# Optimization experiments

Measured on AMD Instinct MI355X. Metric: run time of the kernel, lower is better.

## Reference

```python
import jax, jax.numpy as jnp
import numpy as np

N_NODES = 100000
N_EDGES = 1600000
IN_DIM = 128
HID = 128
OUT_DIM = 2
NUM_GRAPHS = 64
BN_EPS = 1e-5


def _glorot(key, shape):
    fan_in, fan_out = shape[0], shape[1]
    lim = np.sqrt(6.0 / (fan_in + fan_out))
    return jax.random.uniform(key, shape, jnp.float32, -lim, lim)


def setup_inputs() -> dict:
    key = jax.random.key(0)
    ks = jax.random.split(key, 12)
    x = jax.random.normal(ks[0], (N_NODES, IN_DIM), jnp.float32)
    edge_index = jax.random.randint(ks[1], (2, N_EDGES), 0, N_NODES, jnp.int64)
    batch = jnp.sort(jax.random.randint(ks[2], (N_NODES,), 0, NUM_GRAPHS, jnp.int64))
    return {
        "x": x,
        "edge_index": edge_index,
        "batch": batch,
        "W1": _glorot(ks[3], (IN_DIM, HID)), "b1": jnp.zeros((HID,), jnp.float32),
        "g1": jnp.ones((HID,), jnp.float32), "be1": jnp.zeros((HID,), jnp.float32),
        "W2": _glorot(ks[4], (HID, HID)), "b2": jnp.zeros((HID,), jnp.float32),
        "g2": jnp.ones((HID,), jnp.float32), "be2": jnp.zeros((HID,), jnp.float32),
        "Wc1": _glorot(ks[5], (HID, HID // 2)), "bc1": jnp.zeros((HID // 2,), jnp.float32),
        "Wc2": _glorot(ks[6], (HID // 2, OUT_DIM)), "bc2": jnp.zeros((OUT_DIM,), jnp.float32),
    }


def gcn_conv(x, src, dst, W, b):
    # PyG GCNConv: add self-loops, symmetric deg^{-1/2} normalization
    n = x.shape[0]
    loop = jnp.arange(n, dtype=src.dtype)
    s = jnp.concatenate([src, loop])
    d = jnp.concatenate([dst, loop])
    deg = jax.ops.segment_sum(jnp.ones_like(d, dtype=x.dtype), d, num_segments=n)
    dinv = jnp.where(deg > 0, jax.lax.rsqrt(deg), 0.0)
    xw = x @ W  # [N, out]
    msgs = xw[s] * (dinv[s] * dinv[d])[:, None]  # [E+N, out]
    out = jax.ops.segment_sum(msgs, d, num_segments=n)
    return out + b


def batchnorm(x, gamma, beta):
    mean = jnp.mean(x, axis=0)
    var = jnp.mean(jnp.square(x - mean), axis=0)  # biased, as torch BN
    return (x - mean) * jax.lax.rsqrt(var + BN_EPS) * gamma + beta


def reference(x, edge_index, batch, W1, b1, g1, be1, W2, b2, g2, be2, Wc1, bc1, Wc2, bc2):
    src, dst = edge_index[0], edge_index[1]
    x = jnp.nan_to_num(x, nan=0.0)
    # layer 1: GCNConv -> BN -> ReLU (dropout = identity in eval)
    h = jax.nn.relu(batchnorm(gcn_conv(x, src, dst, W1, b1), g1, be1))
    # layer 2
    h = jax.nn.relu(batchnorm(gcn_conv(h, src, dst, W2, b2), g2, be2))
    # global mean pool per graph
    sums = jax.ops.segment_sum(h, batch, num_segments=NUM_GRAPHS)
    counts = jax.ops.segment_sum(jnp.ones((h.shape[0],), h.dtype), batch, num_segments=NUM_GRAPHS)
    pooled = sums / jnp.maximum(counts, 1.0)[:, None]  # [G, HID]
    # classifier MLP
    z = jax.nn.relu(pooled @ Wc1 + bc1)
    out = z @ Wc2 + bc2
    return jnp.nan_to_num(out, nan=0.0)
```

## Files before the change

kernel.cpp:

```cpp
#include <hip/hip_runtime.h>

typedef unsigned int uint;
typedef unsigned short ushort;

#define HID 128
#define NGRAPH 64

typedef __attribute__((ext_vector_type(8))) short short8;
typedef __attribute__((ext_vector_type(4))) float floatx4;

__device__ __forceinline__ float bflo(uint w){ return __uint_as_float(w<<16); }
__device__ __forceinline__ float bfhi(uint w){ return __uint_as_float(w & 0xffff0000u); }
__device__ __forceinline__ float bf2f(ushort u){ return __uint_as_float(((uint)u)<<16); }
__device__ __forceinline__ ushort f2bf(float f){
  uint u = __float_as_uint(f);
  u = u + 0x7fffu + ((u>>16)&1u);
  return (ushort)(u>>16);
}
__device__ __forceinline__ uint pack2(float a, float b){
  return (uint)f2bf(a) | ((uint)f2bf(b)<<16);
}
__device__ __forceinline__ float nanz(float v){ return (v==v) ? v : 0.f; }

__device__ __forceinline__ int bat(const int* b, int i, int is64){
  return is64 ? b[2*(size_t)i] : b[i];
}

__global__ void k_prep(int* __restrict__ cnt, float* __restrict__ stats1,
                       float* __restrict__ stats2, float* __restrict__ pooled,
                       uint* __restrict__ xwzero, int NN,
                       const int* __restrict__ ei, int* __restrict__ flags,
                       const float* __restrict__ W1, const float* __restrict__ W2,
                       ushort* __restrict__ wt1, ushort* __restrict__ wt2){
  int bid = blockIdx.x;
  if (bid < 512){
    int i = bid*256 + threadIdx.x;
    for (int t = i; t < NN; t += 512*256) cnt[t] = 0;
    if (i < 256){ stats1[i] = 0.f; stats2[i] = 0.f; }
    if (i < NGRAPH*HID) pooled[i] = 0.f;
    if (i < 64) xwzero[i] = 0u;
    if (bid == 0 && threadIdx.x < 64){
      int t = threadIdx.x;
      bool nz = (ei[2*t + 1] != 0) || (ei[2*(t+64) + 1] != 0);
      unsigned long long m = __ballot(nz);
      if (t == 0) flags[1] = (m == 0ULL) ? 1 : 0;
    }
  } else {
    int b = bid - 512;
    const float* W  = (b & 1) ? W2  : W1;
    ushort*      Wt = (b & 1) ? wt2 : wt1;
    int base = (b >> 1)*4096;
    for (int o = base + threadIdx.x; o < base + 4096; o += 256){
      int j    = o & 7;
      int lane = (o >> 3) & 63;
      int ct   = (o >> 9) & 7;
      int ks   = o >> 12;
      int k = ks*32 + (lane >> 4)*8 + j;
      int n = ct*16 + (lane & 15);
      Wt[o] = f2bf(W[(size_t)k*HID + n]);
    }
  }
}

__global__ void k_sentinel(ushort* out, int n){
  int i = blockIdx.x*blockDim.x + threadIdx.x;
  if (i < n) out[i] = 0x429A;
}

__global__ __launch_bounds__(256) void k_compacthist(const int* __restrict__ ei,
    const int* __restrict__ flags, int* __restrict__ src32, int* __restrict__ dst32,
    int* __restrict__ cnt, int E, int NN){
  int is64 = flags[1];
  int i = blockIdx.x*256 + (int)threadIdx.x;
  int stride = gridDim.x*256;
  if (is64){
    for (int e = i; e < E; e += stride){
      int s = ei[2*(size_t)e];
      int d = ei[2*((size_t)E + e)];
      src32[e] = s; dst32[e] = d;
      if ((uint)d < (uint)NN && (uint)s < (uint)NN) atomicAdd(&cnt[d], 1);
    }
  } else {
    for (int e = i; e < E; e += stride){
      int s = ei[e];
      int d = ei[(size_t)E + e];
      src32[e] = s; dst32[e] = d;
      if ((uint)d < (uint)NN && (uint)s < (uint)NN) atomicAdd(&cnt[d], 1);
    }
  }
}

__global__ void k_scan1(const int* __restrict__ cnt, int* __restrict__ partials,
                        float* __restrict__ dinv, int NN){
  int t = threadIdx.x;
  int base = blockIdx.x*1024 + t*4;
  int v0=0,v1=0,v2=0,v3=0;
  if (base + 3 < NN){ int4 v = *(const int4*)(cnt + base); v0=v.x; v1=v.y; v2=v.z; v3=v.w; }
  else {
    if (base+0 < NN) v0 = cnt[base+0];
    if (base+1 < NN) v1 = cnt[base+1];
    if (base+2 < NN) v2 = cnt[base+2];
    if (base+3 < NN) v3 = cnt[base+3];
  }
  if (base+0 < NN) dinv[base+0] = rsqrtf((float)(v0+1));
  if (base+1 < NN) dinv[base+1] = rsqrtf((float)(v1+1));
  if (base+2 < NN) dinv[base+2] = rsqrtf((float)(v2+1));
  if (base+3 < NN) dinv[base+3] = rsqrtf((float)(v3+1));
  __shared__ int red[256];
  red[t] = v0+v1+v2+v3;
  __syncthreads();
  for (int off=128; off>0; off>>=1){
    if (t < off) red[t] += red[t+off];
    __syncthreads();
  }
  if (t==0) partials[blockIdx.x] = red[0];
}

__global__ void k_scan3(const int* __restrict__ cnt, const int* __restrict__ partials,
                        int* __restrict__ offs, int* __restrict__ cursor, int NN){
  int t = threadIdx.x;
  __shared__ int red2[256];
  int lp = 0;
  for (int i = t; i < (int)blockIdx.x; i += 256) lp += partials[i];
  red2[t] = lp;
  __syncthreads();
  for (int off=128; off>0; off>>=1){
    if (t < off) red2[t] += red2[t+off];
    __syncthreads();
  }
  int pbase = red2[0];
  if (t == 0 && blockIdx.x == gridDim.x-1)
    offs[NN] = pbase + partials[blockIdx.x];
  __syncthreads();

  int base = blockIdx.x*1024 + t*4;
  int v0=0,v1=0,v2=0,v3=0;
  if (base + 3 < NN){ int4 v = *(const int4*)(cnt + base); v0=v.x; v1=v.y; v2=v.z; v3=v.w; }
  else {
    if (base+0 < NN) v0 = cnt[base+0];
    if (base+1 < NN) v1 = cnt[base+1];
    if (base+2 < NN) v2 = cnt[base+2];
    if (base+3 < NN) v3 = cnt[base+3];
  }
  int tsum = v0+v1+v2+v3;
  __shared__ int sc[256];
  sc[t] = tsum;
  __syncthreads();
  for (int off=1; off<256; off<<=1){
    int val = (t >= off) ? sc[t-off] : 0;
    __syncthreads();
    sc[t] += val;
    __syncthreads();
  }
  int run = pbase + sc[t] - tsum;
  if (base+0 < NN){ offs[base+0] = run; cursor[base+0] = run; run += v0; }
  if (base+1 < NN){ offs[base+1] = run; cursor[base+1] = run; run += v1; }
  if (base+2 < NN){ offs[base+2] = run; cursor[base+2] = run; run += v2; }
  if (base+3 < NN){ offs[base+3] = run; cursor[base+3] = run; run += v3; }
}


#define NCHUNK 256

__global__ __launch_bounds__(256) void k_scatter(const int* __restrict__ src32,
    const int* __restrict__ dst32, int* __restrict__ cursor,
    int* __restrict__ srclist, int E, int NN){
  int part  = blockIdx.x & 7;
  int chunk = blockIdx.x >> 3;
  int p0 = (int)(((long long)NN *  part   ) >> 3);
  int p1 = (int)(((long long)NN * (part+1)) >> 3);
  int per = (E + NCHUNK - 1) / NCHUNK;
  int e0 = chunk * per;
  int e1 = e0 + per; if (e1 > E) e1 = E;
  for (int e = e0 + (int)threadIdx.x; e < e1; e += 256){
    int d = dst32[e];
    if (d >= p0 && d < p1){
      int s = src32[e];
      if ((uint)s < (uint)NN)
        srclist[atomicAdd(&cursor[d], 1)] = s;
    }
  }
}


__global__ __launch_bounds__(256) void k_gemm1(const float* __restrict__ A,
    const ushort* __restrict__ Wt, const float* __restrict__ dinv,
    ushort* __restrict__ O, int NN){
  __shared__ ushort wlds[16384];
  int tid = threadIdx.x;
  {
    const uint4* s = (const uint4*)Wt;
    uint4* d = (uint4*)wlds;
    #pragma unroll
    for (int i = 0; i < 8; i++) d[tid + i*256] = s[tid + i*256];
  }
  __syncthreads();
  int wave = tid >> 6, lane = tid & 63, m = lane & 15, q = lane >> 4;
  int rowbase = blockIdx.x*64 + wave*16;
  int ar = rowbase + m; if (ar >= NN) ar = NN-1;
  const float* arow = A + (size_t)ar*HID;
  short8 af[4];
  #pragma unroll
  for (int ks=0; ks<4; ks++){
    int kb = ks*32 + q*8;
    float4 f0 = *(const float4*)(arow + kb);
    float4 f1 = *(const float4*)(arow + kb + 4);
    short8 t;
    t[0]=(short)f2bf(nanz(f0.x)); t[1]=(short)f2bf(nanz(f0.y));
    t[2]=(short)f2bf(nanz(f0.z)); t[3]=(short)f2bf(nanz(f0.w));
    t[4]=(short)f2bf(nanz(f1.x)); t[5]=(short)f2bf(nanz(f1.y));
    t[6]=(short)f2bf(nanz(f1.z)); t[7]=(short)f2bf(nanz(f1.w));
    af[ks] = t;
  }
  floatx4 acc[8];
  #pragma unroll
  for (int ct=0; ct<8; ct++) acc[ct] = (floatx4){0.f,0.f,0.f,0.f};
  #pragma unroll
  for (int ks=0; ks<4; ks++){
    #pragma unroll
    for (int ct=0; ct<8; ct++){
      short8 bfrag = *(const short8*)&wlds[(((ks*8+ct)*64) + lane)*8];
      acc[ct] = __builtin_amdgcn_mfma_f32_16x16x32_bf16(af[ks], bfrag, acc[ct], 0, 0, 0);
    }
  }
  float dv[4];
  #pragma unroll
  for (int i=0;i<4;i++){ int r = rowbase + q*4 + i; dv[i] = (r < NN) ? dinv[r] : 0.f; }
  #pragma unroll
  for (int ct=0; ct<8; ct++){
    #pragma unroll
    for (int i=0;i<4;i++){
      int r = rowbase + q*4 + i;
      if (r < NN) O[(size_t)r*HID + ct*16 + m] = f2bf(acc[ct][i]*dv[i]);
    }
  }
}


__global__ __launch_bounds__(256) void k_gemm2(const uint* __restrict__ agg,
    const float* __restrict__ stats, const float* __restrict__ gam,
    const float* __restrict__ bet, const ushort* __restrict__ Wt,
    const float* __restrict__ dinv, ushort* __restrict__ O, int NN, float invn){
  __shared__ ushort wlds[16384];
  __shared__ float cA[128], cB[128];
  int tid = threadIdx.x;
  {
    const uint4* s = (const uint4*)Wt;
    uint4* d = (uint4*)wlds;
    #pragma unroll
    for (int i = 0; i < 8; i++) d[tid + i*256] = s[tid + i*256];
    if (tid < 128){
      float sm = stats[tid], sq = stats[128+tid];
      float mean = sm*invn;
      float var = fmaxf(sq*invn - mean*mean, 0.f);
      float a = gam[tid] * rsqrtf(var + 1e-5f);
      cA[tid] = a;
      cB[tid] = bet[tid] - mean*a;
    }
  }
  __syncthreads();
  int wave = tid >> 6, lane = tid & 63, m = lane & 15, q = lane >> 4;
  int rowbase = blockIdx.x*64 + wave*16;
  int ar = rowbase + m; if (ar >= NN) ar = NN-1;
  const uint* arow = agg + (size_t)ar*64;
  short8 af[4];
  #pragma unroll
  for (int ks=0; ks<4; ks++){
    int kb = ks*32 + q*8;
    uint4 u = *(const uint4*)(arow + (kb >> 1));
    short8 t;
    uint uw[4] = {u.x, u.y, u.z, u.w};
    #pragma unroll
    for (int p=0; p<4; p++){
      int k0 = kb + 2*p;
      float v0 = fmaxf(cA[k0]  *bflo(uw[p]) + cB[k0],   0.f);
      float v1 = fmaxf(cA[k0+1]*bfhi(uw[p]) + cB[k0+1], 0.f);
      t[2*p]   = (short)f2bf(v0);
      t[2*p+1] = (short)f2bf(v1);
    }
    af[ks] = t;
  }
  floatx4 acc[8];
  #pragma unroll
  for (int ct=0; ct<8; ct++) acc[ct] = (floatx4){0.f,0.f,0.f,0.f};
  #pragma unroll
  for (int ks=0; ks<4; ks++){
    #pragma unroll
    for (int ct=0; ct<8; ct++){
      short8 bfrag = *(const short8*)&wlds[(((ks*8+ct)*64) + lane)*8];
      acc[ct] = __builtin_amdgcn_mfma_f32_16x16x32_bf16(af[ks], bfrag, acc[ct], 0, 0, 0);
    }
  }
  float dv[4];
  #pragma unroll
  for (int i=0;i<4;i++){ int r = rowbase + q*4 + i; dv[i] = (r < NN) ? dinv[r] : 0.f; }
  #pragma unroll
  for (int ct=0; ct<8; ct++){
    #pragma unroll
    for (int i=0;i<4;i++){
      int r = rowbase + q*4 + i;
      if (r < NN) O[(size_t)r*HID + ct*16 + m] = f2bf(acc[ct][i]*dv[i]);
    }
  }
}


__global__ __launch_bounds__(256) void k_agg(const uint* __restrict__ xw,
    const int* __restrict__ offs, const int* __restrict__ srclist,
    const float* __restrict__ dinv, uint* __restrict__ agg,
    float* __restrict__ stats, int NN){
  __shared__ float lstat[256];
  lstat[threadIdx.x] = 0.f;
  __syncthreads();
  int wib = threadIdx.x >> 6;
  int lane = threadIdx.x & 63;
  int wid = blockIdx.x*4 + wib;
  int nw = gridDim.x*4;
  float s0=0.f, s1=0.f, q0=0.f, q1=0.f;
  for (int n = wid; n < NN; n += nw){
    int lo = offs[n], hi = offs[n+1];
    float dvn = dinv[n];
    float a0 = 0.f, a1 = 0.f;
    for (int base = lo; base < hi; base += 64){
      int c = hi - base; if (c > 64) c = 64;
      int sidx = (lane < c) ? srclist[base + lane] : NN;
      for (int jb = 0; jb < c; jb += 8){
        uint w[8];
        #pragma unroll
        for (int t = 0; t < 8; t++){
          int sj = __shfl(sidx, jb + t, 64);
          w[t] = xw[(size_t)sj*64 + lane];
        }
        #pragma unroll
        for (int t = 0; t < 8; t++){
          a0 += bflo(w[t]);
          a1 += bfhi(w[t]);
        }
      }
    }
    uint wsf = xw[(size_t)n*64 + lane];
    a0 = (a0 + bflo(wsf)) * dvn;
    a1 = (a1 + bfhi(wsf)) * dvn;
    agg[(size_t)n*64 + lane] = pack2(a0, a1);
    s0 += a0; s1 += a1; q0 += a0*a0; q1 += a1*a1;
  }
  int ch = lane*2;
  atomicAdd(&lstat[ch],       s0);
  atomicAdd(&lstat[ch+1],     s1);
  atomicAdd(&lstat[128+ch],   q0);
  atomicAdd(&lstat[128+ch+1], q1);
  __syncthreads();
  atomicAdd(&stats[threadIdx.x], lstat[threadIdx.x]);
}


#define PSPLIT 16

__global__ __launch_bounds__(256) void k_pool(const uint* __restrict__ agg32,
    const int* __restrict__ batch, const float* __restrict__ stats,
    const float* __restrict__ gam, const float* __restrict__ bet,
    float* __restrict__ pooled, int* __restrict__ counts,
    int NN, const int* __restrict__ flags, float invn){
  int is64 = flags[1];
  __shared__ int bounds[2];
  __shared__ float cA[128], cB[128];
  int g  = blockIdx.x;
  int si = blockIdx.y;
  int tid = threadIdx.x;
  if (tid < 128){
    float sm = stats[tid], sq = stats[128+tid];
    float mean = sm*invn;
    float var = fmaxf(sq*invn - mean*mean, 0.f);
    float a = gam[tid] * rsqrtf(var + 1e-5f);
    cA[tid] = a;
    cB[tid] = bet[tid] - mean*a;
  }
  if (tid == 0){
    int lo=0, hi=NN;
    while (lo<hi){ int mid=(lo+hi)>>1; if (bat(batch,mid,is64) < g) lo=mid+1; else hi=mid; }
    bounds[0] = lo;
    int lo2=lo, hi2=NN;
    while (lo2<hi2){ int mid=(lo2+hi2)>>1; if (bat(batch,mid,is64) < g+1) lo2=mid+1; else hi2=mid; }
    bounds[1] = lo2;
    if (si == 0) counts[g] = hi2 - lo;
  }
  __syncthreads();
  int lo = bounds[0], hi = bounds[1];
  int cnt = hi - lo;
  int chunk = (cnt + PSPLIT - 1) / PSPLIT;
  int s = lo + si*chunk;
  int e = s + chunk; if (e > hi) e = hi;
  int lane = tid & 63, rg = tid >> 6;
  int ch = lane*2;
  float a0c = cA[ch],   b0c = cB[ch];
  float a1c = cA[ch+1], b1c = cB[ch+1];
  float acc0 = 0.f, acc1 = 0.f;
  for (int r = s + rg; r < e; r += 4){
    uint w = agg32[(size_t)r*64 + lane];
    acc0 += fmaxf(a0c*bflo(w) + b0c, 0.f);
    acc1 += fmaxf(a1c*bfhi(w) + b1c, 0.f);
  }
  __shared__ float red[512];
  red[tid] = acc0;
  red[256+tid] = acc1;
  __syncthreads();
  if (tid < 64){
    float s0 = red[tid] + red[tid+64] + red[tid+128] + red[tid+192];
    float s1 = red[256+tid] + red[320+tid] + red[384+tid] + red[448+tid];
    atomicAdd(&pooled[g*HID + ch],     s0);
    atomicAdd(&pooled[g*HID + ch + 1], s1);
  }
}


__global__ __launch_bounds__(128) void k_mlp(const float* __restrict__ pooled,
    const int* __restrict__ counts, const float* __restrict__ Wc1,
    const float* __restrict__ bc1, const float* __restrict__ Wc2,
    const float* __restrict__ bc2, float* __restrict__ out){
  int g = blockIdx.x;
  __shared__ float P[HID];
  __shared__ float Z[64];
  int tid = threadIdx.x;
  {
    float c = (float)counts[g];
    P[tid] = pooled[g*HID + tid] / fmaxf(c, 1.f);
  }
  __syncthreads();
  if (tid < 64){
    float acc = bc1[tid];
    for (int k = 0; k < HID; k++) acc += P[k] * Wc1[k*64 + tid];
    Z[tid] = fmaxf(acc, 0.f);
  }
  __syncthreads();
  if (tid < 2){
    float acc = bc2[tid];
    for (int k = 0; k < 64; k++) acc += Z[k] * Wc2[k*2 + tid];
    out[g*2 + tid] = nanz(acc);
  }
}

extern "C" void kernel_launch(void* const* d_in, const int* in_sizes, int n_in,
                              void* d_out, int out_size, void* d_ws, size_t ws_size,
                              hipStream_t stream){
  const float* x   = (const float*)d_in[0];
  const int*   ei  = (const int*)d_in[1];
  const int* batch = (const int*)d_in[2];
  const float* W1  = (const float*)d_in[3];
  const float* g1  = (const float*)d_in[5];
  const float* be1 = (const float*)d_in[6];
  const float* W2  = (const float*)d_in[7];
  const float* g2  = (const float*)d_in[9];
  const float* be2 = (const float*)d_in[10];
  const float* Wc1 = (const float*)d_in[11];
  const float* bc1 = (const float*)d_in[12];
  const float* Wc2 = (const float*)d_in[13];
  const float* bc2 = (const float*)d_in[14];

  const int NN = in_sizes[2];
  const int E  = in_sizes[1] / 2;

  char* p = (char*)d_ws;
  auto carve = [&](size_t bytes)->char*{
    char* r = p; p += (bytes + 255) & ~(size_t)255; return r;
  };
  int NPART = (NN + 1023)/1024;
  int*   flags    = (int*)  carve(64*4);
  int*   cnt      = (int*)  carve((size_t)NN*4);
  int*   cursor   = (int*)  carve(((size_t)NN+1)*4);
  int*   offs     = (int*)  carve(((size_t)NN+1)*4);
  int*   partials = (int*)  carve((size_t)NPART*4);
  int*   srclist  = (int*)  carve((size_t)E*4);
  int*   src32    = (int*)  carve((size_t)E*4);
  int*   dst32    = (int*)  carve((size_t)E*4);
  float* dinv     = (float*)carve((size_t)NN*4);
  float* stats1   = (float*)carve(256*4);
  float* stats2   = (float*)carve(256*4);
  float* pooled   = (float*)carve((size_t)NGRAPH*HID*4);
  int*   counts   = (int*)  carve(NGRAPH*4);
  ushort* wt1     = (ushort*)carve(16384*2);
  ushort* wt2     = (ushort*)carve(16384*2);
  ushort* xw      = (ushort*)carve(((size_t)NN+1)*HID*2);
  ushort* agg     = (ushort*)carve((size_t)NN*HID*2);
  if ((size_t)(p - (char*)d_ws) > ws_size){
    k_sentinel<<<(out_size+255)/256, 256, 0, stream>>>((ushort*)d_out, out_size);
    return;
  }

  const float invn = 1.f/(float)NN;

  k_prep       <<<520, 256, 0, stream>>>(cnt, stats1, stats2, pooled,
                                         (uint*)(xw + (size_t)NN*HID), NN, ei, flags,
                                         W1, W2, wt1, wt2);
  k_compacthist<<<512, 256, 0, stream>>>(ei, flags, src32, dst32, cnt, E, NN);
  k_scan1      <<<NPART, 256, 0, stream>>>(cnt, partials, dinv, NN);
  k_scan3      <<<NPART, 256, 0, stream>>>(cnt, partials, offs, cursor, NN);
  k_scatter    <<<NCHUNK*8, 256, 0, stream>>>(src32, dst32, cursor, srclist, E, NN);

  int gblocks = (NN + 63)/64;
  k_gemm1<<<gblocks, 256, 0, stream>>>(x, wt1, dinv, xw, NN);
  k_agg  <<<2048, 256, 0, stream>>>((const uint*)xw, offs, srclist, dinv, (uint*)agg, stats1, NN);
  k_gemm2<<<gblocks, 256, 0, stream>>>((const uint*)agg, stats1, g1, be1, wt2, dinv, xw, NN, invn);
  k_agg  <<<2048, 256, 0, stream>>>((const uint*)xw, offs, srclist, dinv, (uint*)agg, stats2, NN);
  k_pool <<<dim3(NGRAPH, PSPLIT), 256, 0, stream>>>((const uint*)agg, batch, stats2, g2, be2,
                                                    pooled, counts, NN, flags, invn);
  k_mlp  <<<NGRAPH, 128, 0, stream>>>(pooled, counts, Wc1, bc1, Wc2, bc2, (float*)d_out);
}
```

Measured before the change: 526.5 us.

## Fuse scatter into gemm1 launch and stage agg gathers through LDS direct loads

```diff
diff --git a/kernel.cpp b/kernel.cpp
--- a/kernel.cpp
+++ b/kernel.cpp
@@ -8,6 +8,9 @@
 
 typedef __attribute__((ext_vector_type(8))) short short8;
 typedef __attribute__((ext_vector_type(4))) float floatx4;
+
+typedef const __attribute__((address_space(1))) unsigned int* gas_u32p;
+typedef __attribute__((address_space(3))) unsigned int* las_u32p;
 
 __device__ __forceinline__ float bflo(uint w){ return __uint_as_float(w<<16); }
 __device__ __forceinline__ float bfhi(uint w){ return __uint_as_float(w & 0xffff0000u); }
@@ -162,39 +165,31 @@
 
 #define NCHUNK 256
 
-__global__ __launch_bounds__(256) void k_scatter(const int* __restrict__ src32,
-    const int* __restrict__ dst32, int* __restrict__ cursor,
-    int* __restrict__ srclist, int E, int NN){
-  int part  = blockIdx.x & 7;
-  int chunk = blockIdx.x >> 3;
-  int p0 = (int)(((long long)NN *  part   ) >> 3);
-  int p1 = (int)(((long long)NN * (part+1)) >> 3);
-  int per = (E + NCHUNK - 1) / NCHUNK;
-  int e0 = chunk * per;
-  int e1 = e0 + per; if (e1 > E) e1 = E;
-  for (int e = e0 + (int)threadIdx.x; e < e1; e += 256){
-    int d = dst32[e];
-    if (d >= p0 && d < p1){
-      int s = src32[e];
-      if ((uint)s < (uint)NN)
-        srclist[atomicAdd(&cursor[d], 1)] = s;
-    }
-  }
-}
-
-
-__global__ __launch_bounds__(256) void k_gemm1(const float* __restrict__ A,
+__global__ __launch_bounds__(256) void k_scatgemm1(const float* __restrict__ A,
     const ushort* __restrict__ Wt, const float* __restrict__ dinv,
-    ushort* __restrict__ O, int NN){
-  __shared__ ushort wlds[16384];
+    ushort* __restrict__ O, int NN,
+    const int* __restrict__ src32, const int* __restrict__ dst32,
+    int* __restrict__ cursor, int* __restrict__ srclist, int E, int gblocks){
+  if ((int)blockIdx.x >= gblocks){
+    int b = blockIdx.x - gblocks;
+    int part  = b & 7;
+    int chunk = b >> 3;
+    int p0 = (int)(((long long)NN *  part   ) >> 3);
+    int p1 = (int)(((long long)NN * (part+1)) >> 3);
+    int per = (E + NCHUNK - 1) / NCHUNK;
+    int e0 = chunk * per;
+    int e1 = e0 + per; if (e1 > E) e1 = E;
+    for (int e = e0 + (int)threadIdx.x; e < e1; e += 256){
+      int d = dst32[e];
+      if (d >= p0 && d < p1){
+        int s = src32[e];
+        if ((uint)s < (uint)NN)
+          srclist[atomicAdd(&cursor[d], 1)] = s;
+      }
+    }
+    return;
+  }
   int tid = threadIdx.x;
-  {
-    const uint4* s = (const uint4*)Wt;
-    uint4* d = (uint4*)wlds;
-    #pragma unroll
-    for (int i = 0; i < 8; i++) d[tid + i*256] = s[tid + i*256];
-  }
-  __syncthreads();
   int wave = tid >> 6, lane = tid & 63, m = lane & 15, q = lane >> 4;
   int rowbase = blockIdx.x*64 + wave*16;
   int ar = rowbase + m; if (ar >= NN) ar = NN-1;
@@ -219,7 +214,7 @@
   for (int ks=0; ks<4; ks++){
     #pragma unroll
     for (int ct=0; ct<8; ct++){
-      short8 bfrag = *(const short8*)&wlds[(((ks*8+ct)*64) + lane)*8];
+      short8 bfrag = *(const short8*)&Wt[(((ks*8+ct)*64) + lane)*8];
       acc[ct] = __builtin_amdgcn_mfma_f32_16x16x32_bf16(af[ks], bfrag, acc[ct], 0, 0, 0);
     }
   }
@@ -305,15 +300,19 @@
 }
 
 
+#define AGG_ROWS 16
+
 __global__ __launch_bounds__(256) void k_agg(const uint* __restrict__ xw,
     const int* __restrict__ offs, const int* __restrict__ srclist,
     const float* __restrict__ dinv, uint* __restrict__ agg,
     float* __restrict__ stats, int NN){
   __shared__ float lstat[256];
+  __shared__ uint rowbuf[4][AGG_ROWS*64];
   lstat[threadIdx.x] = 0.f;
   __syncthreads();
   int wib = threadIdx.x >> 6;
   int lane = threadIdx.x & 63;
+  uint* mybuf = &rowbuf[wib][0];
   int wid = blockIdx.x*4 + wib;
   int nw = gridDim.x*4;
   float s0=0.f, s1=0.f, q0=0.f, q1=0.f;
@@ -324,17 +323,20 @@
     for (int base = lo; base < hi; base += 64){
       int c = hi - base; if (c > 64) c = 64;
       int sidx = (lane < c) ? srclist[base + lane] : NN;
-      for (int jb = 0; jb < c; jb += 8){
-        uint w[8];
+      for (int jb = 0; jb < c; jb += AGG_ROWS){
         #pragma unroll
-        for (int t = 0; t < 8; t++){
+        for (int t = 0; t < AGG_ROWS; t++){
           int sj = __shfl(sidx, jb + t, 64);
-          w[t] = xw[(size_t)sj*64 + lane];
+          __builtin_amdgcn_global_load_lds(
+              (gas_u32p)(xw + (size_t)sj*64 + lane),
+              (las_u32p)&mybuf[t*64], 4, 0, 0);
         }
+        __builtin_amdgcn_s_waitcnt(0);
         #pragma unroll
-        for (int t = 0; t < 8; t++){
-          a0 += bflo(w[t]);
-          a1 += bfhi(w[t]);
+        for (int t = 0; t < AGG_ROWS; t++){
+          uint w = mybuf[t*64 + lane];
+          a0 += bflo(w);
+          a1 += bfhi(w);
         }
       }
     }
@@ -487,6 +489,7 @@
   }
 
   const float invn = 1.f/(float)NN;
+  int gblocks = (NN + 63)/64;
 
   k_prep       <<<520, 256, 0, stream>>>(cnt, stats1, stats2, pooled,
                                          (uint*)(xw + (size_t)NN*HID), NN, ei, flags,
@@ -494,10 +497,8 @@
   k_compacthist<<<512, 256, 0, stream>>>(ei, flags, src32, dst32, cnt, E, NN);
   k_scan1      <<<NPART, 256, 0, stream>>>(cnt, partials, dinv, NN);
   k_scan3      <<<NPART, 256, 0, stream>>>(cnt, partials, offs, cursor, NN);
-  k_scatter    <<<NCHUNK*8, 256, 0, stream>>>(src32, dst32, cursor, srclist, E, NN);
-
-  int gblocks = (NN + 63)/64;
-  k_gemm1<<<gblocks, 256, 0, stream>>>(x, wt1, dinv, xw, NN);
+  k_scatgemm1  <<<gblocks + NCHUNK*8, 256, 0, stream>>>(x, wt1, dinv, xw, NN,
+                                                        src32, dst32, cursor, srclist, E, gblocks);
   k_agg  <<<2048, 256, 0, stream>>>((const uint*)xw, offs, srclist, dinv, (uint*)agg, stats1, NN);
   k_gemm2<<<gblocks, 256, 0, stream>>>((const uint*)agg, stats1, g1, be1, wt2, dinv, xw, NN, invn);
   k_agg  <<<2048, 256, 0, stream>>>((const uint*)xw, offs, srclist, dinv, (uint*)agg, stats2, NN);
```

After: 549.4 us. +4.3%, slower.
